# Kernel tuning notes

Hardware: AMD Instinct MI355X
Metric: run time of the kernel (lower is better)

The kernel has to match this reference:

```python
import jax, jax.numpy as jnp
import numpy as np

NUM_ATOMS = 40000
NUM_EDGES = 640000
FAN_IN = 128
NFM = 128
FAN_OUT = 128


def setup_inputs() -> dict:
    key = jax.random.key(0)
    k1, k2, k3, k4, k5, k6, k7 = jax.random.split(key, 7)
    x = jax.random.normal(k1, (NUM_ATOMS, FAN_IN), dtype=jnp.float32)
    w_ij = jax.random.normal(k2, (NUM_EDGES, NFM), dtype=jnp.float32)
    seg_i = jnp.sort(jax.random.randint(k3, (NUM_EDGES,), 0, NUM_ATOMS))
    idx_j = jax.random.randint(k4, (NUM_EDGES,), 0, NUM_ATOMS)
    # learned params: in2fac (no bias), fac2out (bias)
    W_in = jax.random.normal(k5, (FAN_IN, NFM), dtype=jnp.float32) / np.sqrt(FAN_IN)
    W_out = jax.random.normal(k6, (NFM, FAN_OUT), dtype=jnp.float32) / np.sqrt(NFM)
    b_out = jax.random.normal(k7, (FAN_OUT,), dtype=jnp.float32) * 0.01
    return {"x": x, "w_ij": w_ij, "seg_i": seg_i, "idx_j": idx_j,
            "seg_i_sum": NUM_ATOMS, "W_in": W_in, "W_out": W_out, "b_out": b_out}


def reference(x, w_ij, seg_i, idx_j, seg_i_sum, W_in, W_out, b_out):
    # in2fac: Dense without bias  (num_atoms, nFM)
    f = x @ W_in
    # gather features of atom j per interaction  (num_edges, nFM)
    f_j = jnp.take(f, idx_j, axis=0)
    # elementwise filter multiply
    wf = w_ij * f_j
    # segment-sum pool over interactions of each atom i  (num_atoms, nFM)
    conv = jax.ops.segment_sum(wf, seg_i, num_segments=seg_i_sum)
    # fac2out: Dense with bias, activation=None
    return conv @ W_out + b_out
```

## Files before the change

### kernel.cpp

```cpp
#include <hip/hip_runtime.h>

#define NUM_ATOMS 40000
#define NUM_EDGES 640000

typedef float f2v __attribute__((ext_vector_type(2)));

__global__ void k_rowstart(const int* __restrict__ seg, int* __restrict__ rs) {
  const int i = blockIdx.x * blockDim.x + threadIdx.x;
  if (i > NUM_ATOMS) return;
  int lo = 0, hi = NUM_EDGES;
  while (lo < hi) {
    const int mid = (lo + hi) >> 1;
    if (seg[mid] < i) lo = mid + 1; else hi = mid;
  }
  rs[i] = lo;
}

__global__ __launch_bounds__(512, 2) void k_gemm128(
    const float* __restrict__ A, const float* __restrict__ W,
    const float* __restrict__ bias, float* __restrict__ out) {
  __shared__ float AT[128 * 128];
  __shared__ float Wl[128 * 128];
  const int t = threadIdx.x;
  const int m0 = blockIdx.x * 128;

  {
    const float4* Wg = (const float4*)W;
    float4* Ws = (float4*)Wl;
#pragma unroll
    for (int i = 0; i < 8; ++i) Ws[t + i * 512] = Wg[t + i * 512];
  }
  {
    const int m = t & 127;
    const int kq = t >> 7;
    int mg = m0 + m;
    if (mg >= NUM_ATOMS) mg = NUM_ATOMS - 1;
    const float4* ag = (const float4*)(A + (size_t)mg * 128);
#pragma unroll
    for (int i = 0; i < 8; ++i) {
      const int k4 = kq + i * 4;
      const float4 v = ag[k4];
      const int k = k4 * 4;
      AT[(k + 0) * 128 + m] = v.x;
      AT[(k + 1) * 128 + m] = v.y;
      AT[(k + 2) * 128 + m] = v.z;
      AT[(k + 3) * 128 + m] = v.w;
    }
  }
  __syncthreads();

  const int tx = t & 31;
  const int ty = t >> 5;

  float binit[4] = {0.f, 0.f, 0.f, 0.f};
  if (bias != nullptr) {
    const float2 bb0 = ((const float2*)bias)[tx];
    const float2 bb1 = ((const float2*)bias)[32 + tx];
    binit[0] = bb0.x; binit[1] = bb0.y; binit[2] = bb1.x; binit[3] = bb1.y;
  }
  float acc[8][4];
#pragma unroll
  for (int i = 0; i < 8; ++i)
#pragma unroll
    for (int j = 0; j < 4; ++j) acc[i][j] = binit[j];

#pragma unroll 4
  for (int k = 0; k < 128; ++k) {
    const float4 a0 = *(const float4*)&AT[k * 128 + 4 * ty];
    const float4 a1 = *(const float4*)&AT[k * 128 + 64 + 4 * ty];
    const float2 b0 = *(const float2*)&Wl[k * 128 + 2 * tx];
    const float2 b1 = *(const float2*)&Wl[k * 128 + 64 + 2 * tx];
    const float av[8] = {a0.x, a0.y, a0.z, a0.w, a1.x, a1.y, a1.z, a1.w};
    const float bv[4] = {b0.x, b0.y, b1.x, b1.y};
#pragma unroll
    for (int i = 0; i < 8; ++i)
#pragma unroll
      for (int j = 0; j < 4; ++j) acc[i][j] += av[i] * bv[j];
  }

#pragma unroll
  for (int i = 0; i < 8; ++i) {
    const int m = (i < 4) ? (4 * ty + i) : (64 + 4 * ty + (i - 4));
    const int mg = m0 + m;
    if (mg < NUM_ATOMS) {
      float2* o = (float2*)(out + (size_t)mg * 128);
      o[tx]      = make_float2(acc[i][0], acc[i][1]);
      o[32 + tx] = make_float2(acc[i][2], acc[i][3]);
    }
  }
}

__global__ __launch_bounds__(256) void k_conv(
    const float* __restrict__ f, const float* __restrict__ w_ij,
    const int* __restrict__ idx_j, const int* __restrict__ rs,
    float* __restrict__ conv) {
  const int wv = threadIdx.x >> 6;
  const int l = threadIdx.x & 63;
  const int a = blockIdx.x * 4 + wv;

  const int e0 = rs[a];
  const int e1 = rs[a + 1];
  float accx = 0.f, accy = 0.f;

  for (int base = e0; base < e1; base += 32) {
    const int n = min(32, e1 - base);
    const int nm1 = n - 1;
    int j = 0;
    if (l < n) j = __builtin_nontemporal_load(idx_j + base + l);

    f2v wr[32];
    float2 fr[32];
#pragma unroll
    for (int g = 0; g < 4; ++g) {
      if (n > g * 8) {
#pragma unroll
        for (int k = g * 8; k < g * 8 + 8; ++k) {
          const int kk = min(k, nm1);
          wr[k] = __builtin_nontemporal_load(
              (const f2v*)(w_ij + (size_t)(base + kk) * 128) + l);
        }
      }
    }
#pragma unroll
    for (int g = 0; g < 4; ++g) {
      if (n > g * 8) {
#pragma unroll
        for (int k = g * 8; k < g * 8 + 8; ++k) {
          const int kk = min(k, nm1);
          const int jk = __shfl(j, kk);
          fr[k] = ((const float2*)(f + (size_t)jk * 128))[l];
        }
      }
    }
#pragma unroll
    for (int g = 0; g < 4; ++g) {
      if (n > g * 8) {
#pragma unroll
        for (int k = g * 8; k < g * 8 + 8; ++k) {
          if (k < n) {
            accx += wr[k].x * fr[k].x;
            accy += wr[k].y * fr[k].y;
          }
        }
      }
    }
  }
  ((float2*)(conv + (size_t)a * 128))[l] = make_float2(accx, accy);
}

extern "C" void kernel_launch(void* const* d_in, const int* in_sizes, int n_in,
                              void* d_out, int out_size, void* d_ws, size_t ws_size,
                              hipStream_t stream) {
  const float* x    = (const float*)d_in[0];
  const float* w_ij = (const float*)d_in[1];
  const int*   seg  = (const int*)d_in[2];
  const int*   idxj = (const int*)d_in[3];
  const float* Win  = (const float*)d_in[5];
  const float* Wout = (const float*)d_in[6];
  const float* bout = (const float*)d_in[7];
  float* out = (float*)d_out;

  float* f    = (float*)d_ws;
  float* conv = (float*)((char*)d_ws + (size_t)NUM_ATOMS * 128 * sizeof(float));
  int*   rs   = (int*)((char*)d_ws + 2 * (size_t)NUM_ATOMS * 128 * sizeof(float));

  k_rowstart<<<(NUM_ATOMS + 1 + 255) / 256, 256, 0, stream>>>(seg, rs);
  k_gemm128<<<(NUM_ATOMS + 127) / 128, 512, 0, stream>>>(x, Win, nullptr, f);
  k_conv<<<NUM_ATOMS / 4, 256, 0, stream>>>(f, w_ij, idxj, rs, conv);
  k_gemm128<<<(NUM_ATOMS + 127) / 128, 512, 0, stream>>>(conv, Wout, bout, out);
}
```

Measured before the change: 546.9 us.

## Fuse segment-sum convolution with output dense layer in a persistent kernel

Merges the gather-multiply-segment-sum kernel and the output GEMM into one persistent kernel. Each wave computes one atom's pooled row, stages it in shared memory, and multiplies it by W_out held in LDS, adding the bias. This removes the conv intermediate buffer round trip and one launch. In exchange, occupancy drops to a fixed grid of 256 blocks with large LDS use, and the output GEMM becomes a per-wave scalar GEMV that is bound by LDS reads.

Measured after the change: 589.2 us. +7.7%, slower.

```diff
diff --git a/kernel.cpp b/kernel.cpp
--- a/kernel.cpp
+++ b/kernel.cpp
@@ -90,62 +90,89 @@
   }
 }
 
-__global__ __launch_bounds__(256) void k_conv(
+__global__ __launch_bounds__(512, 2) void k_conv_out(
     const float* __restrict__ f, const float* __restrict__ w_ij,
     const int* __restrict__ idx_j, const int* __restrict__ rs,
-    float* __restrict__ conv) {
-  const int wv = threadIdx.x >> 6;
-  const int l = threadIdx.x & 63;
-  const int a = blockIdx.x * 4 + wv;
+    const float* __restrict__ Wout, const float* __restrict__ bout,
+    float* __restrict__ out) {
+  __shared__ float Ws[128 * 128];
+  __shared__ float cs[8][128];
+  const int t = threadIdx.x;
+  const int wv = t >> 6;
+  const int l = t & 63;
 
-  const int e0 = rs[a];
-  const int e1 = rs[a + 1];
-  float accx = 0.f, accy = 0.f;
+  {
+    const float4* Wg = (const float4*)Wout;
+    float4* Wl4 = (float4*)Ws;
+#pragma unroll
+    for (int i = 0; i < 8; ++i) Wl4[t + i * 512] = Wg[t + i * 512];
+  }
+  __syncthreads();
 
-  for (int base = e0; base < e1; base += 32) {
-    const int n = min(32, e1 - base);
-    const int nm1 = n - 1;
-    int j = 0;
-    if (l < n) j = __builtin_nontemporal_load(idx_j + base + l);
+  const float b0 = bout[l];
+  const float b1 = bout[64 + l];
 
-    f2v wr[32];
-    float2 fr[32];
+  for (int a = blockIdx.x * 8 + wv; a < NUM_ATOMS; a += 2048) {
+    const int e0 = rs[a];
+    const int e1 = rs[a + 1];
+    float accx = 0.f, accy = 0.f;
+
+    for (int base = e0; base < e1; base += 32) {
+      const int n = min(32, e1 - base);
+      const int nm1 = n - 1;
+      int j = 0;
+      if (l < n) j = __builtin_nontemporal_load(idx_j + base + l);
+
+      f2v wr[32];
+      float2 fr[32];
 #pragma unroll
-    for (int g = 0; g < 4; ++g) {
-      if (n > g * 8) {
+      for (int g = 0; g < 4; ++g) {
+        if (n > g * 8) {
 #pragma unroll
-        for (int k = g * 8; k < g * 8 + 8; ++k) {
-          const int kk = min(k, nm1);
-          wr[k] = __builtin_nontemporal_load(
-              (const f2v*)(w_ij + (size_t)(base + kk) * 128) + l);
+          for (int k = g * 8; k < g * 8 + 8; ++k) {
+            const int kk = min(k, nm1);
+            wr[k] = __builtin_nontemporal_load(
+                (const f2v*)(w_ij + (size_t)(base + kk) * 128) + l);
+          }
         }
       }
-    }
 #pragma unroll
-    for (int g = 0; g < 4; ++g) {
-      if (n > g * 8) {
+      for (int g = 0; g < 4; ++g) {
+        if (n > g * 8) {
 #pragma unroll
-        for (int k = g * 8; k < g * 8 + 8; ++k) {
-          const int kk = min(k, nm1);
-          const int jk = __shfl(j, kk);
-          fr[k] = ((const float2*)(f + (size_t)jk * 128))[l];
+          for (int k = g * 8; k < g * 8 + 8; ++k) {
+            const int kk = min(k, nm1);
+            const int jk = __shfl(j, kk);
+            fr[k] = ((const float2*)(f + (size_t)jk * 128))[l];
+          }
         }
       }
-    }
 #pragma unroll
-    for (int g = 0; g < 4; ++g) {
-      if (n > g * 8) {
+      for (int g = 0; g < 4; ++g) {
+        if (n > g * 8) {
 #pragma unroll
-        for (int k = g * 8; k < g * 8 + 8; ++k) {
-          if (k < n) {
-            accx += wr[k].x * fr[k].x;
-            accy += wr[k].y * fr[k].y;
+          for (int k = g * 8; k < g * 8 + 8; ++k) {
+            if (k < n) {
+              accx += wr[k].x * fr[k].x;
+              accy += wr[k].y * fr[k].y;
+            }
           }
         }
       }
     }
+
+    ((float2*)cs[wv])[l] = make_float2(accx, accy);
+
+    float o0 = b0, o1 = b1;
+#pragma unroll 8
+    for (int k = 0; k < 128; ++k) {
+      const float ck = cs[wv][k];
+      o0 += ck * Ws[k * 128 + l];
+      o1 += ck * Ws[k * 128 + 64 + l];
+    }
+    out[(size_t)a * 128 + l] = o0;
+    out[(size_t)a * 128 + 64 + l] = o1;
   }
-  ((float2*)(conv + (size_t)a * 128))[l] = make_float2(accx, accy);
 }
 
 extern "C" void kernel_launch(void* const* d_in, const int* in_sizes, int n_in,
@@ -160,12 +187,10 @@
   const float* bout = (const float*)d_in[7];
   float* out = (float*)d_out;
 
-  float* f    = (float*)d_ws;
-  float* conv = (float*)((char*)d_ws + (size_t)NUM_ATOMS * 128 * sizeof(float));
-  int*   rs   = (int*)((char*)d_ws + 2 * (size_t)NUM_ATOMS * 128 * sizeof(float));
+  float* f  = (float*)d_ws;
+  int*   rs = (int*)((char*)d_ws + (size_t)NUM_ATOMS * 128 * sizeof(float));
 
   k_rowstart<<<(NUM_ATOMS + 1 + 255) / 256, 256, 0, stream>>>(seg, rs);
   k_gemm128<<<(NUM_ATOMS + 127) / 128, 512, 0, stream>>>(x, Win, nullptr, f);
-  k_conv<<<NUM_ATOMS / 4, 256, 0, stream>>>(f, w_ij, idxj, rs, conv);
-  k_gemm128<<<(NUM_ATOMS + 127) / 128, 512, 0, stream>>>(conv, Wout, bout, out);
+  k_conv_out<<<256, 512, 0, stream>>>(f, w_ij, idxj, rs, Wout, bout, out);
 }
```
